# Kernel optimization log

Hardware: AMD Instinct MI355X
Metric: run time of the kernel (lower is better)

## Reference

```python
import jax, jax.numpy as jnp
import numpy as np

N, F, E = 100000, 128, 1600000


def setup_inputs() -> dict:
    key = jax.random.key(0)
    ks = jax.random.split(key, 10)
    s = 1.0 / np.sqrt(F)
    return {
        "x": jax.random.normal(ks[0], (N, F), jnp.float32),
        "edge_index": jax.random.randint(ks[1], (2, E), 0, N),
        "edge_weight": jax.random.uniform(ks[2], (E,), jnp.float32),
        # EvolveGCNO initial weight (1, F, F) -> squeezed to (F, F)
        "initial_weight": jax.random.normal(ks[3], (F, F), jnp.float32) * s,
        # torch.nn.GRU(F, F) params, gate order (r, z, n)
        "gru_w_ih": jax.random.uniform(ks[4], (3 * F, F), jnp.float32, -s, s),
        "gru_w_hh": jax.random.uniform(ks[5], (3 * F, F), jnp.float32, -s, s),
        "gru_b_ih": jax.random.uniform(ks[6], (3 * F,), jnp.float32, -s, s),
        "gru_b_hh": jax.random.uniform(ks[7], (3 * F,), jnp.float32, -s, s),
        # Linear(F, 1)
        "lin_w": jax.random.uniform(ks[8], (1, F), jnp.float32, -s, s),
        "lin_b": jax.random.uniform(ks[9], (1,), jnp.float32, -s, s),
    }


def _evolve_weight(W0, w_ih, w_hh, b_ih, b_hh):
    # One GRU step: input = W0 rows (batch=F), hidden = W0 rows (first call of EvolveGCNO)
    gi = W0 @ w_ih.T + b_ih  # (F, 3F)
    gh = W0 @ w_hh.T + b_hh
    i_r, i_z, i_n = jnp.split(gi, 3, axis=-1)
    h_r, h_z, h_n = jnp.split(gh, 3, axis=-1)
    r = jax.nn.sigmoid(i_r + h_r)
    z = jax.nn.sigmoid(i_z + h_z)
    n = jnp.tanh(i_n + r * h_n)
    return (1.0 - z) * n + z * W0  # (F, F)


def reference(x, edge_index, edge_weight, initial_weight, gru_w_ih, gru_w_hh,
              gru_b_ih, gru_b_hh, lin_w, lin_b):
    W = _evolve_weight(initial_weight, gru_w_ih, gru_w_hh, gru_b_ih, gru_b_hh)
    n_nodes = x.shape[0]
    row, col = edge_index[0], edge_index[1]  # source, target
    # gcn_norm: add self loops (weight 1), sym-normalize D^-1/2 (A+I) D^-1/2
    loop = jnp.arange(n_nodes)
    row = jnp.concatenate([row, loop])
    col = jnp.concatenate([col, loop])
    w = jnp.concatenate([edge_weight, jnp.ones((n_nodes,), x.dtype)])
    deg = jax.ops.segment_sum(w, col, num_segments=n_nodes)
    dinv = jnp.where(deg > 0, jax.lax.rsqrt(deg), 0.0)
    norm = dinv[row] * w * dinv[col]  # (E+N,)
    xw = x @ W  # (N, F)
    # gather at sources, weighted scatter-add at targets
    h = jax.ops.segment_sum(norm[:, None] * xw[row], col, num_segments=n_nodes)
    h = jax.nn.relu(h)
    return (h @ lin_w.T + lin_b)[:, 0]  # (N,)
```

## Files before the change

kernel.cpp:

```cpp
#include <hip/hip_runtime.h>

#define F 128
#define DEG_SCALE 16777216.0f
#define DEG_INV   (1.0f / 16777216.0f)
#define BUCK_BITS 7
#define BUCK_COLS 128
#define CAP 2304
#define EPT 8
#define WB_STRIDE 136

typedef _Float16 half8 __attribute__((ext_vector_type(8)));
typedef float f32x4 __attribute__((ext_vector_type(4)));

__global__ __launch_bounds__(256) void init_kernel(
    int* __restrict__ cursor, int NZ, int NBUK,
    const float* __restrict__ W0, const float* __restrict__ wih,
    const float* __restrict__ whh, const float* __restrict__ bih,
    const float* __restrict__ bhh, float* __restrict__ W) {
  __shared__ float w0row[2][F];
  int b = blockIdx.x;
  if (b < NZ) {
    int i = b * 256 + threadIdx.x;
    if (i < NBUK) cursor[i] = 0;
    return;
  }
  int half = threadIdx.x >> 7;
  int j = threadIdx.x & 127;
  int i = (b - NZ) * 2 + half;
  w0row[half][j] = W0[i * F + j];
  __syncthreads();
  float ar = 0, az = 0, an = 0, br = 0, bz = 0, bn = 0;
  const float* wi_r = wih + (size_t)j * F;
  const float* wi_z = wih + (size_t)(j + F) * F;
  const float* wi_n = wih + (size_t)(j + 2 * F) * F;
  const float* wh_r = whh + (size_t)j * F;
  const float* wh_z = whh + (size_t)(j + F) * F;
  const float* wh_n = whh + (size_t)(j + 2 * F) * F;
#pragma unroll 4
  for (int k = 0; k < F; ++k) {
    float a = w0row[half][k];
    ar = fmaf(a, wi_r[k], ar);
    az = fmaf(a, wi_z[k], az);
    an = fmaf(a, wi_n[k], an);
    br = fmaf(a, wh_r[k], br);
    bz = fmaf(a, wh_z[k], bz);
    bn = fmaf(a, wh_n[k], bn);
  }
  float gr = ar + bih[j] + br + bhh[j];
  float gz = az + bih[j + F] + bz + bhh[j + F];
  float r = 1.f / (1.f + expf(-gr));
  float z = 1.f / (1.f + expf(-gz));
  float n = tanhf(an + bih[j + 2 * F] + r * (bn + bhh[j + 2 * F]));
  W[i * F + j] = (1.f - z) * n + z * w0row[half][j];
}

__global__ __launch_bounds__(1024) void gemm_bin(
    const float* __restrict__ x, const float* __restrict__ W,
    _Float16* __restrict__ xwh, int N, int GB,
    const int* __restrict__ row, const int* __restrict__ col,
    const float* __restrict__ ew, int* __restrict__ cursor,
    uint2* __restrict__ binned, int E, int NBUK) {
  __shared__ _Float16 Wb[F * WB_STRIDE];
  __shared__ int cnt[1024];
  __shared__ int base[1024];
  int t = threadIdx.x;

  if ((int)blockIdx.x >= GB) {
    cnt[t] = 0;
    __syncthreads();
    int e0 = ((int)blockIdx.x - GB) * (1024 * EPT) + t;
    int cc[EPT];
    int lrank[EPT];
#pragma unroll
    for (int k = 0; k < EPT; ++k) {
      int e = e0 + k * 1024;
      if (e < E) {
        cc[k] = col[e];
        lrank[k] = atomicAdd(&cnt[cc[k] >> BUCK_BITS], 1);
      } else cc[k] = -1;
    }
    __syncthreads();
    if (t < NBUK) {
      int c = cnt[t];
      base[t] = c ? atomicAdd(&cursor[t], c) : 0;
    }
    __syncthreads();
#pragma unroll
    for (int k = 0; k < EPT; ++k) {
      if (cc[k] >= 0) {
        int e = e0 + k * 1024;
        int b = cc[k] >> BUCK_BITS;
        int pos = base[b] + lrank[k];
        if (pos < CAP) {
          unsigned cl = (unsigned)(cc[k] & (BUCK_COLS - 1));
          binned[(size_t)b * CAP + pos] =
              make_uint2((unsigned)row[e] | (cl << 17), __float_as_uint(ew[e]));
        }
      }
    }
    return;
  }

  for (int idx = t; idx < F * F; idx += 1024) {
    int k = idx >> 7, n = idx & 127;
    Wb[n * WB_STRIDE + k] = (_Float16)W[idx];
  }
  __syncthreads();

  int lane = t & 63, wave = t >> 6;
  int ln = lane & 15, q = lane >> 4;
  int rowb = blockIdx.x * 256 + wave * 16;
  int i = rowb + ln;
  int iclamp = (i < N) ? i : N - 1;
  const float* xp = x + (size_t)iclamp * F + q * 8;

  half8 a[4];
#pragma unroll
  for (int tt = 0; tt < 4; ++tt) {
    float4 v0 = *(const float4*)(xp + 32 * tt);
    float4 v1 = *(const float4*)(xp + 32 * tt + 4);
    half8 av;
    av[0] = (_Float16)v0.x; av[1] = (_Float16)v0.y;
    av[2] = (_Float16)v0.z; av[3] = (_Float16)v0.w;
    av[4] = (_Float16)v1.x; av[5] = (_Float16)v1.y;
    av[6] = (_Float16)v1.z; av[7] = (_Float16)v1.w;
    a[tt] = av;
  }

  f32x4 acc[8];
#pragma unroll
  for (int nt = 0; nt < 8; ++nt) acc[nt] = (f32x4){0.f, 0.f, 0.f, 0.f};

#pragma unroll
  for (int nt = 0; nt < 8; ++nt) {
#pragma unroll
    for (int tt = 0; tt < 4; ++tt) {
      half8 bfrag = *(const half8*)&Wb[(nt * 16 + ln) * WB_STRIDE + tt * 32 + q * 8];
      acc[nt] = __builtin_amdgcn_mfma_f32_16x16x32_f16(a[tt], bfrag, acc[nt], 0, 0, 0);
    }
  }

#pragma unroll
  for (int nt = 0; nt < 8; ++nt) {
#pragma unroll
    for (int r = 0; r < 4; ++r) {
      int rowi = rowb + q * 4 + r;
      if (rowi < N) xwh[(size_t)rowi * F + nt * 16 + ln] = (_Float16)acc[nt][r];
    }
  }
}

__global__ __launch_bounds__(256) void csr_kernel(
    const uint2* __restrict__ binned, const int* __restrict__ cursor,
    int* __restrict__ offs, float* __restrict__ dinv,
    uint2* __restrict__ pairs, int N, int NBUK) {
  __shared__ unsigned long long acc[BUCK_COLS];
  __shared__ float dinvL[BUCK_COLS];
  __shared__ int sc[BUCK_COLS];
  __shared__ int woff[BUCK_COLS];
  __shared__ int wsum[4];
  __shared__ uint2 sorted[CAP + BUCK_COLS];
  int b = blockIdx.x;
  int tid = threadIdx.x;
  if (tid < BUCK_COLS) acc[tid] = 0ull;
  int partial = 0;
  for (int i = tid; i < b; i += 256) partial += cursor[i];
#pragma unroll
  for (int m = 32; m; m >>= 1) partial += __shfl_xor(partial, m);
  if ((tid & 63) == 0) wsum[tid >> 6] = partial;
  __syncthreads();
  int bstart = b * BUCK_COLS + wsum[0] + wsum[1] + wsum[2] + wsum[3];

  int cnt = cursor[b];
  if (cnt > CAP) cnt = CAP;
  const uint2* src = binned + (size_t)b * CAP;
  for (int i = tid; i < cnt; i += 256) {
    uint2 rec = src[i];
    int cl = rec.x >> 17;
    unsigned fx = (unsigned)(__uint_as_float(rec.y) * DEG_SCALE);
    atomicAdd(&acc[cl], ((unsigned long long)1 << 32) | (unsigned long long)fx);
  }
  __syncthreads();
  int node0 = b * BUCK_COLS;
  int cvt1 = 0;
  if (tid < BUCK_COLS) {
    int node = node0 + tid;
    if (node < N) {
      unsigned long long pk = acc[tid];
      cvt1 = (int)(pk >> 32) + 1;
      float deg = (float)(unsigned)(pk & 0xffffffffull) * DEG_INV;
      float dv = rsqrtf(deg + 1.0f);
      dinvL[tid] = dv;
      dinv[node] = dv;
    }
    sc[tid] = cvt1;
  }
  __syncthreads();
  for (int off = 1; off < BUCK_COLS; off <<= 1) {
    int x = 0;
    if (tid < BUCK_COLS && tid >= off) x = sc[tid - off];
    __syncthreads();
    if (tid < BUCK_COLS) sc[tid] += x;
    __syncthreads();
  }
  if (tid < BUCK_COLS) {
    int node = node0 + tid;
    if (node < N) {
      int rel0 = sc[tid] - cvt1;
      offs[node] = bstart + rel0;
      sorted[rel0] = make_uint2((unsigned)node << 8, __float_as_uint(dinvL[tid]));
      woff[tid] = rel0 + 1;
    }
  }
  __syncthreads();
  for (int i = tid; i < cnt; i += 256) {
    uint2 rec = src[i];
    int cl = rec.x >> 17;
    unsigned r = rec.x & 0x1ffffu;
    float wp = __uint_as_float(rec.y) * dinvL[cl];
    int pos = atomicAdd(&woff[cl], 1);
    sorted[pos] = make_uint2(r << 8, __float_as_uint(wp));
  }
  __syncthreads();
  int tot = sc[BUCK_COLS - 1];
  for (int i = tid; i < tot; i += 256) pairs[bstart + i] = sorted[i];
  if (b == NBUK - 1 && tid == 0) offs[N] = bstart + tot;
}

__global__ __launch_bounds__(256) void gather_out(
    const uint2* __restrict__ pairs, const int* __restrict__ offs,
    const float* __restrict__ dinv, const char* __restrict__ xwb,
    const float* __restrict__ linw, const float* __restrict__ linb,
    float* __restrict__ out, int N) {
  int wave = threadIdx.x >> 6;
  int lane = threadIdx.x & 63;
  int node = blockIdx.x * 4 + wave;
  if (node >= N) return;
  int c = lane & 15;
  int q = lane >> 4;

  const char* xb = xwb + (c << 4);
  float acc[8];
#pragma unroll
  for (int j = 0; j < 8; ++j) acc[j] = 0.f;

  half8 zero8 = {0, 0, 0, 0, 0, 0, 0, 0};
  uint2 p1 = make_uint2(0u, 0u), p2 = p1, p3 = p1;
  half8 x1 = zero8, x2 = zero8, x3 = zero8;
  float d1 = 0.f, d2 = 0.f, d3 = 0.f;

  int start = offs[node], end = offs[node + 1];
  for (int it = start + q; it < end; it += 16) {
    uint2 p0 = pairs[it];
    half8 x0 = *(const half8*)(xb + p0.x);
    float d0 = dinv[p0.x >> 8];
    bool v1 = it + 4 < end, v2 = it + 8 < end, v3 = it + 12 < end;
    if (v1) {
      p1 = pairs[it + 4];
      x1 = *(const half8*)(xb + p1.x);
      d1 = dinv[p1.x >> 8];
    }
    if (v2) {
      p2 = pairs[it + 8];
      x2 = *(const half8*)(xb + p2.x);
      d2 = dinv[p2.x >> 8];
    }
    if (v3) {
      p3 = pairs[it + 12];
      x3 = *(const half8*)(xb + p3.x);
      d3 = dinv[p3.x >> 8];
    }
    float n0 = __uint_as_float(p0.y) * d0;
    float n1 = v1 ? __uint_as_float(p1.y) * d1 : 0.f;
    float n2 = v2 ? __uint_as_float(p2.y) * d2 : 0.f;
    float n3 = v3 ? __uint_as_float(p3.y) * d3 : 0.f;
#pragma unroll
    for (int j = 0; j < 8; ++j) acc[j] = fmaf(n0, (float)x0[j], acc[j]);
#pragma unroll
    for (int j = 0; j < 8; ++j) acc[j] = fmaf(n1, (float)x1[j], acc[j]);
#pragma unroll
    for (int j = 0; j < 8; ++j) acc[j] = fmaf(n2, (float)x2[j], acc[j]);
#pragma unroll
    for (int j = 0; j < 8; ++j) acc[j] = fmaf(n3, (float)x3[j], acc[j]);
  }

#pragma unroll
  for (int j = 0; j < 8; ++j) {
    acc[j] += __shfl_xor(acc[j], 16);
    acc[j] += __shfl_xor(acc[j], 32);
  }

  const float4* lw4 = (const float4*)linw;
  float4 la = lw4[c * 2];
  float4 lb = lw4[c * 2 + 1];
  float p = fmaxf(acc[0], 0.f) * la.x + fmaxf(acc[1], 0.f) * la.y +
            fmaxf(acc[2], 0.f) * la.z + fmaxf(acc[3], 0.f) * la.w +
            fmaxf(acc[4], 0.f) * lb.x + fmaxf(acc[5], 0.f) * lb.y +
            fmaxf(acc[6], 0.f) * lb.z + fmaxf(acc[7], 0.f) * lb.w;
#pragma unroll
  for (int m = 8; m; m >>= 1) p += __shfl_xor(p, m);

  if (lane == 0) out[node] = p + linb[0];
}

extern "C" void kernel_launch(void* const* d_in, const int* in_sizes, int n_in,
                              void* d_out, int out_size, void* d_ws, size_t ws_size,
                              hipStream_t stream) {
  const float* x    = (const float*)d_in[0];
  const int*   ei   = (const int*)d_in[1];
  const float* ew   = (const float*)d_in[2];
  const float* W0   = (const float*)d_in[3];
  const float* wih  = (const float*)d_in[4];
  const float* whh  = (const float*)d_in[5];
  const float* bih  = (const float*)d_in[6];
  const float* bhh  = (const float*)d_in[7];
  const float* linw = (const float*)d_in[8];
  const float* linb = (const float*)d_in[9];

  int N = in_sizes[0] / F;
  int E = in_sizes[2];
  const int* row = ei;
  const int* col = ei + E;
  int NBUK = (N + BUCK_COLS - 1) / BUCK_COLS;
  int total = E + N;

  char* p = (char*)d_ws;
  auto alloc = [&](size_t bytes) {
    char* q = p;
    p += (bytes + 255) & ~(size_t)255;
    return q;
  };
  float*    W      = (float*)alloc((size_t)F * F * 4);
  int*      cursor = (int*)alloc((size_t)NBUK * 4);
  float*    dinv   = (float*)alloc((size_t)N * 4);
  int*      offs   = (int*)alloc(((size_t)N + 1) * 4);
  uint2*    binned = (uint2*)alloc((size_t)NBUK * CAP * 8);
  uint2*    pairs  = (uint2*)alloc((size_t)total * 8);
  _Float16* xwh    = (_Float16*)alloc((size_t)N * F * 2);

  int NZ = (NBUK + 255) / 256;
  init_kernel<<<NZ + 64, 256, 0, stream>>>(cursor, NZ, NBUK, W0, wih, whh, bih, bhh, W);

  int GB = (N + 255) / 256;
  int BB = (E + 1024 * EPT - 1) / (1024 * EPT);
  gemm_bin<<<GB + BB, 1024, 0, stream>>>(x, W, xwh, N, GB,
                                         row, col, ew, cursor, binned, E, NBUK);

  csr_kernel<<<NBUK, 256, 0, stream>>>(binned, cursor, offs, dinv, pairs, N, NBUK);

  gather_out<<<(N + 3) / 4, 256, 0, stream>>>(pairs, offs, dinv, (const char*)xwh,
                                              linw, linb, (float*)d_out, N);
}
```

Baseline: 257.0 us.

## Precompute full edge norm in CSR build and accumulate gather in packed fp16

The CSR build is split into a degree kernel and a fill kernel, so the fill pass can fold dinv[source] into each edge weight and store the complete symmetric norm. The gather then no longer does a dependent per-edge dinv lookup. It also loads all four unrolled edges unconditionally, relying on padding added at the end of pairs, and accumulates in packed fp16 vector FMAs instead of scalar fp32. This trades an extra kernel launch and a second pass over binned data for a cheaper gather inner loop, at the risk of fp16 accumulation error.

Result: no change. 258.4 us (+0.6%).

```diff
diff --git a/kernel.cpp b/kernel.cpp
--- a/kernel.cpp
+++ b/kernel.cpp
@@ -150,27 +150,14 @@
   }
 }
 
-__global__ __launch_bounds__(256) void csr_kernel(
+__global__ __launch_bounds__(256) void csr_deg(
     const uint2* __restrict__ binned, const int* __restrict__ cursor,
-    int* __restrict__ offs, float* __restrict__ dinv,
-    uint2* __restrict__ pairs, int N, int NBUK) {
+    float* __restrict__ dinv, int* __restrict__ cnts, int N) {
   __shared__ unsigned long long acc[BUCK_COLS];
-  __shared__ float dinvL[BUCK_COLS];
-  __shared__ int sc[BUCK_COLS];
-  __shared__ int woff[BUCK_COLS];
-  __shared__ int wsum[4];
-  __shared__ uint2 sorted[CAP + BUCK_COLS];
   int b = blockIdx.x;
   int tid = threadIdx.x;
   if (tid < BUCK_COLS) acc[tid] = 0ull;
-  int partial = 0;
-  for (int i = tid; i < b; i += 256) partial += cursor[i];
-#pragma unroll
-  for (int m = 32; m; m >>= 1) partial += __shfl_xor(partial, m);
-  if ((tid & 63) == 0) wsum[tid >> 6] = partial;
-  __syncthreads();
-  int bstart = b * BUCK_COLS + wsum[0] + wsum[1] + wsum[2] + wsum[3];
-
+  __syncthreads();
   int cnt = cursor[b];
   if (cnt > CAP) cnt = CAP;
   const uint2* src = binned + (size_t)b * CAP;
@@ -181,17 +168,43 @@
     atomicAdd(&acc[cl], ((unsigned long long)1 << 32) | (unsigned long long)fx);
   }
   __syncthreads();
+  if (tid < BUCK_COLS) {
+    int node = b * BUCK_COLS + tid;
+    if (node < N) {
+      unsigned long long pk = acc[tid];
+      float deg = (float)(unsigned)(pk & 0xffffffffull) * DEG_INV;
+      dinv[node] = rsqrtf(deg + 1.0f);
+      cnts[node] = (int)(pk >> 32);
+    }
+  }
+}
+
+__global__ __launch_bounds__(256) void csr_fill(
+    const uint2* __restrict__ binned, const int* __restrict__ cursor,
+    const int* __restrict__ cnts, const float* __restrict__ dinv,
+    int* __restrict__ offs, uint2* __restrict__ pairs, int N, int NBUK) {
+  __shared__ float dinvL[BUCK_COLS];
+  __shared__ int sc[BUCK_COLS];
+  __shared__ int woff[BUCK_COLS];
+  __shared__ int wsum[4];
+  __shared__ uint2 sorted[CAP + BUCK_COLS];
+  int b = blockIdx.x;
+  int tid = threadIdx.x;
+  int partial = 0;
+  for (int i = tid; i < b; i += 256) partial += min(cursor[i], CAP);
+#pragma unroll
+  for (int m = 32; m; m >>= 1) partial += __shfl_xor(partial, m);
+  if ((tid & 63) == 0) wsum[tid >> 6] = partial;
+  __syncthreads();
+  int bstart = b * BUCK_COLS + wsum[0] + wsum[1] + wsum[2] + wsum[3];
+
   int node0 = b * BUCK_COLS;
   int cvt1 = 0;
   if (tid < BUCK_COLS) {
     int node = node0 + tid;
     if (node < N) {
-      unsigned long long pk = acc[tid];
-      cvt1 = (int)(pk >> 32) + 1;
-      float deg = (float)(unsigned)(pk & 0xffffffffull) * DEG_INV;
-      float dv = rsqrtf(deg + 1.0f);
-      dinvL[tid] = dv;
-      dinv[node] = dv;
+      cvt1 = cnts[node] + 1;
+      dinvL[tid] = dinv[node];
     }
     sc[tid] = cvt1;
   }
@@ -208,30 +221,36 @@
     if (node < N) {
       int rel0 = sc[tid] - cvt1;
       offs[node] = bstart + rel0;
-      sorted[rel0] = make_uint2((unsigned)node << 8, __float_as_uint(dinvL[tid]));
+      float dv = dinvL[tid];
+      sorted[rel0] = make_uint2((unsigned)node << 8, __float_as_uint(dv * dv));
       woff[tid] = rel0 + 1;
     }
   }
   __syncthreads();
+  int cnt = cursor[b];
+  if (cnt > CAP) cnt = CAP;
+  const uint2* src = binned + (size_t)b * CAP;
   for (int i = tid; i < cnt; i += 256) {
     uint2 rec = src[i];
     int cl = rec.x >> 17;
     unsigned r = rec.x & 0x1ffffu;
-    float wp = __uint_as_float(rec.y) * dinvL[cl];
+    float wp = __uint_as_float(rec.y) * dinvL[cl] * dinv[r];
     int pos = atomicAdd(&woff[cl], 1);
     sorted[pos] = make_uint2(r << 8, __float_as_uint(wp));
   }
   __syncthreads();
   int tot = sc[BUCK_COLS - 1];
   for (int i = tid; i < tot; i += 256) pairs[bstart + i] = sorted[i];
-  if (b == NBUK - 1 && tid == 0) offs[N] = bstart + tot;
+  if (b == NBUK - 1) {
+    if (tid == 0) offs[N] = bstart + tot;
+    if (tid < 16) pairs[bstart + tot + tid] = make_uint2(0u, 0u);
+  }
 }
 
 __global__ __launch_bounds__(256) void gather_out(
     const uint2* __restrict__ pairs, const int* __restrict__ offs,
-    const float* __restrict__ dinv, const char* __restrict__ xwb,
-    const float* __restrict__ linw, const float* __restrict__ linb,
-    float* __restrict__ out, int N) {
+    const char* __restrict__ xwb, const float* __restrict__ linw,
+    const float* __restrict__ linb, float* __restrict__ out, int N) {
   int wave = threadIdx.x >> 6;
   int lane = threadIdx.x & 63;
   int node = blockIdx.x * 4 + wave;
@@ -240,49 +259,38 @@
   int q = lane >> 4;
 
   const char* xb = xwb + (c << 4);
-  float acc[8];
-#pragma unroll
-  for (int j = 0; j < 8; ++j) acc[j] = 0.f;
-
-  half8 zero8 = {0, 0, 0, 0, 0, 0, 0, 0};
-  uint2 p1 = make_uint2(0u, 0u), p2 = p1, p3 = p1;
-  half8 x1 = zero8, x2 = zero8, x3 = zero8;
-  float d1 = 0.f, d2 = 0.f, d3 = 0.f;
+  half8 acca = {0, 0, 0, 0, 0, 0, 0, 0};
+  half8 accb = {0, 0, 0, 0, 0, 0, 0, 0};
 
   int start = offs[node], end = offs[node + 1];
   for (int it = start + q; it < end; it += 16) {
     uint2 p0 = pairs[it];
+    uint2 p1 = pairs[it + 4];
+    uint2 p2 = pairs[it + 8];
+    uint2 p3 = pairs[it + 12];
     half8 x0 = *(const half8*)(xb + p0.x);
-    float d0 = dinv[p0.x >> 8];
-    bool v1 = it + 4 < end, v2 = it + 8 < end, v3 = it + 12 < end;
-    if (v1) {
-      p1 = pairs[it + 4];
-      x1 = *(const half8*)(xb + p1.x);
-      d1 = dinv[p1.x >> 8];
-    }
-    if (v2) {
-      p2 = pairs[it + 8];
-      x2 = *(const half8*)(xb + p2.x);
-      d2 = dinv[p2.x >> 8];
-    }
-    if (v3) {
-      p3 = pairs[it + 12];
-      x3 = *(const half8*)(xb + p3.x);
-      d3 = dinv[p3.x >> 8];
-    }
-    float n0 = __uint_as_float(p0.y) * d0;
-    float n1 = v1 ? __uint_as_float(p1.y) * d1 : 0.f;
-    float n2 = v2 ? __uint_as_float(p2.y) * d2 : 0.f;
-    float n3 = v3 ? __uint_as_float(p3.y) * d3 : 0.f;
-#pragma unroll
-    for (int j = 0; j < 8; ++j) acc[j] = fmaf(n0, (float)x0[j], acc[j]);
-#pragma unroll
-    for (int j = 0; j < 8; ++j) acc[j] = fmaf(n1, (float)x1[j], acc[j]);
-#pragma unroll
-    for (int j = 0; j < 8; ++j) acc[j] = fmaf(n2, (float)x2[j], acc[j]);
-#pragma unroll
-    for (int j = 0; j < 8; ++j) acc[j] = fmaf(n3, (float)x3[j], acc[j]);
-  }
+    half8 x1 = *(const half8*)(xb + p1.x);
+    half8 x2 = *(const half8*)(xb + p2.x);
+    half8 x3 = *(const half8*)(xb + p3.x);
+    float f0 = __uint_as_float(p0.y);
+    float f1 = (it + 4 < end) ? __uint_as_float(p1.y) : 0.f;
+    float f2 = (it + 8 < end) ? __uint_as_float(p2.y) : 0.f;
+    float f3 = (it + 12 < end) ? __uint_as_float(p3.y) : 0.f;
+    _Float16 h0 = (_Float16)f0, h1 = (_Float16)f1;
+    _Float16 h2 = (_Float16)f2, h3 = (_Float16)f3;
+    half8 n0 = {h0, h0, h0, h0, h0, h0, h0, h0};
+    half8 n1 = {h1, h1, h1, h1, h1, h1, h1, h1};
+    half8 n2 = {h2, h2, h2, h2, h2, h2, h2, h2};
+    half8 n3 = {h3, h3, h3, h3, h3, h3, h3, h3};
+    acca += x0 * n0;
+    accb += x1 * n1;
+    acca += x2 * n2;
+    accb += x3 * n3;
+  }
+
+  float acc[8];
+#pragma unroll
+  for (int j = 0; j < 8; ++j) acc[j] = (float)acca[j] + (float)accb[j];
 
 #pragma unroll
   for (int j = 0; j < 8; ++j) {
@@ -333,9 +341,10 @@
   float*    W      = (float*)alloc((size_t)F * F * 4);
   int*      cursor = (int*)alloc((size_t)NBUK * 4);
   float*    dinv   = (float*)alloc((size_t)N * 4);
+  int*      cnts   = (int*)alloc((size_t)N * 4);
   int*      offs   = (int*)alloc(((size_t)N + 1) * 4);
   uint2*    binned = (uint2*)alloc((size_t)NBUK * CAP * 8);
-  uint2*    pairs  = (uint2*)alloc((size_t)total * 8);
+  uint2*    pairs  = (uint2*)alloc(((size_t)total + 16) * 8);
   _Float16* xwh    = (_Float16*)alloc((size_t)N * F * 2);
 
   int NZ = (NBUK + 255) / 256;
@@ -346,8 +355,9 @@
   gemm_bin<<<GB + BB, 1024, 0, stream>>>(x, W, xwh, N, GB,
                                          row, col, ew, cursor, binned, E, NBUK);
 
-  csr_kernel<<<NBUK, 256, 0, stream>>>(binned, cursor, offs, dinv, pairs, N, NBUK);
-
-  gather_out<<<(N + 3) / 4, 256, 0, stream>>>(pairs, offs, dinv, (const char*)xwh,
+  csr_deg<<<NBUK, 256, 0, stream>>>(binned, cursor, dinv, cnts, N);
+  csr_fill<<<NBUK, 256, 0, stream>>>(binned, cursor, cnts, dinv, offs, pairs, N, NBUK);
+
+  gather_out<<<(N + 3) / 4, 256, 0, stream>>>(pairs, offs, (const char*)xwh,
                                               linw, linb, (float*)d_out, N);
 }
```
